# Optimization experiments

Measured on AMD Instinct MI355X. Metric: run time of the kernel, lower is better.

## Reference

```python
import jax, jax.numpy as jnp
import numpy as np

N, E, L, H, C, F, NCLASS, NGRAPH = 50000, 800000, 3, 2, 64, 128, 10, 64
NEG_SLOPE = 0.2


def setup_inputs() -> dict:
    key = jax.random.key(0)
    ks = jax.random.split(key, 8)
    x = jax.random.normal(ks[0], (N, F), dtype=jnp.float32)
    edge_index = jax.random.randint(ks[1], (2, E), 0, N, dtype=jnp.int64)
    batch = jnp.sort(jax.random.randint(ks[2], (N,), 0, NGRAPH, dtype=jnp.int64))
    s = 1.0 / np.sqrt(F)
    W = jax.random.normal(ks[3], (L, F, H * C), dtype=jnp.float32) * s
    att_src = jax.random.normal(ks[4], (L, H, C), dtype=jnp.float32) * s
    att_dst = jax.random.normal(ks[5], (L, H, C), dtype=jnp.float32) * s
    bias = jnp.zeros((L, H * C), dtype=jnp.float32)
    lin_w = jax.random.normal(ks[6], (H * C, NCLASS), dtype=jnp.float32) * s
    lin_b = jnp.zeros((NCLASS,), dtype=jnp.float32)
    return {"x": x, "edge_index": edge_index, "batch": batch, "W": W,
            "att_src": att_src, "att_dst": att_dst, "bias": bias,
            "lin_w": lin_w, "lin_b": lin_b}


def _gat_layer(x, src, dst, w, a_s, a_d, b):
    n = x.shape[0]
    h = (x @ w).reshape(n, H, C)                      # [N,H,C]
    alpha_src = jnp.sum(h * a_s, axis=-1)             # [N,H]
    alpha_dst = jnp.sum(h * a_d, axis=-1)             # [N,H]
    e = jax.nn.leaky_relu(alpha_src[src] + alpha_dst[dst], NEG_SLOPE)  # [E2,H]
    # scatter-softmax over incoming edges of each destination node
    m = jax.ops.segment_max(e, dst, num_segments=n)
    p = jnp.exp(e - m[dst])
    z = jax.ops.segment_sum(p, dst, num_segments=n)
    alpha = p / z[dst]                                # [E2,H]
    msg = h[src] * alpha[:, :, None]                  # [E2,H,C]
    out = jax.ops.segment_sum(msg, dst, num_segments=n)  # [N,H,C]
    return out.reshape(n, H * C) + b


def reference(x, edge_index, batch, W, att_src, att_dst, bias, lin_w, lin_b):
    n = x.shape[0]
    # PyG GATConv default: add self-loops
    loop = jnp.arange(n, dtype=edge_index.dtype)
    src = jnp.concatenate([edge_index[0], loop])
    dst = jnp.concatenate([edge_index[1], loop])
    for l in range(L):
        x = _gat_layer(x, src, dst, W[l], att_src[l], att_dst[l], bias[l])
        x = jax.nn.elu(x)  # activation; dropout/bn inactive (eval, use_bn=False)
    # global mean pool per graph
    sums = jax.ops.segment_sum(x, batch, num_segments=NGRAPH)
    cnt = jax.ops.segment_sum(jnp.ones((n,), x.dtype), batch, num_segments=NGRAPH)
    pooled = sums / jnp.maximum(cnt, 1.0)[:, None]    # [NGRAPH, H*C]
    logits = pooled @ lin_w + lin_b
    return jax.nn.softmax(logits, axis=1)
```

## Files before the change

### kernel.cpp

```cpp
#include <hip/hip_runtime.h>
#include <math.h>

#define NNODES 50000
#define NEDGES 800000
#define NLAYERS 3
#define NHEADS 2
#define NCH 64
#define FDIM 128
#define NCLS 10
#define NGRAPH 64
#define NEG_SLOPE 0.2f
#define NBLK ((NNODES + 255) / 256)
#define GEMMB ((NNODES + 63) / 64)
#define HISTB ((NEDGES + 255) / 256)

#define WAVE_SYNC()                      \
  do {                                   \
    __builtin_amdgcn_wave_barrier();     \
    __asm__ volatile("" ::: "memory");   \
  } while (0)

__device__ __forceinline__ unsigned short f2bf(float f) {
  unsigned int u = __builtin_bit_cast(unsigned int, f);
  unsigned int r = u + 0x7FFFu + ((u >> 16) & 1u);
  return (unsigned short)(r >> 16);
}
__device__ __forceinline__ float bflo(unsigned v) {
  return __builtin_bit_cast(float, v << 16);
}
__device__ __forceinline__ float bfhi(unsigned v) {
  return __builtin_bit_cast(float, v & 0xFFFF0000u);
}


__global__ void k_init(int* __restrict__ deg, float* __restrict__ gsum,
                       float* __restrict__ gcnt) {
  int i = blockIdx.x * 256 + threadIdx.x;
  if (i < NNODES) deg[i] = 1;
  if (i < NGRAPH * FDIM) gsum[i] = 0.f;
  if (i < NGRAPH) gcnt[i] = 0.f;
}

__global__ __launch_bounds__(256) void k_scan1(const int* __restrict__ deg,
                                               int* __restrict__ pre,
                                               int* __restrict__ bsum) {
  __shared__ int ps[256];
  int t = threadIdx.x;
  int i = blockIdx.x * 256 + t;
  int c = (i < NNODES) ? deg[i] : 0;
  ps[t] = c;
  __syncthreads();
  for (int off = 1; off < 256; off <<= 1) {
    int v = (t >= off) ? ps[t - off] : 0;
    __syncthreads();
    ps[t] += v;
    __syncthreads();
  }
  if (i < NNODES) pre[i] = ps[t] - c;
  if (t == 255) bsum[blockIdx.x] = ps[255];
}

__global__ __launch_bounds__(256) void k_scan2(const int* __restrict__ bsum,
                                               int* __restrict__ boff) {
  __shared__ int ps[256];
  int t = threadIdx.x;
  int c = (t < NBLK) ? bsum[t] : 0;
  ps[t] = c;
  __syncthreads();
  for (int off = 1; off < 256; off <<= 1) {
    int v = (t >= off) ? ps[t - off] : 0;
    __syncthreads();
    ps[t] += v;
    __syncthreads();
  }
  if (t < NBLK) boff[t] = ps[t] - c;
}

__global__ void k_scan3(const int* __restrict__ pre,
                        const int* __restrict__ boff,
                        int* __restrict__ row_ptr, int* __restrict__ csr) {
  int i = blockIdx.x * 256 + threadIdx.x;
  if (i < NNODES) {
    int o = pre[i] + boff[i >> 8];
    row_ptr[i] = o;
    csr[o] = i;
  }
  if (i == 0) row_ptr[NNODES] = NEDGES + NNODES;
}

__global__ void k_scatter(const int* __restrict__ ei,
                          const int* __restrict__ row_ptr,
                          const int* __restrict__ rank, int* __restrict__ csr) {
  int e = blockIdx.x * 256 + threadIdx.x;
  if (e < NEDGES) {
    int d = ei[NEDGES + e];
    csr[row_ptr[d] + rank[e]] = ei[e];
  }
}

__device__ __forceinline__ void gemm_body(int blk, const float* __restrict__ X,
                                          const float* __restrict__ Wg,
                                          const float* __restrict__ a_sL,
                                          const float* __restrict__ a_dL,
                                          unsigned* __restrict__ Hb,
                                          float* __restrict__ as_,
                                          float* __restrict__ ad_) {
  __shared__ float Xs[64][33];
  __shared__ float Ws[32][128];
  int t = threadIdx.x;
  int lane = t & 63;
  int row0 = blk * 64;
  int col = (t & 31) * 4;
  int rbase = (t >> 5) * 8;
  float acc[8][4];
#pragma unroll
  for (int i = 0; i < 8; ++i)
#pragma unroll
    for (int j = 0; j < 4; ++j) acc[i][j] = 0.f;

  for (int k0 = 0; k0 < 128; k0 += 32) {
    {
      int xr = t >> 2, xk = (t & 3) * 8;
      int gr = row0 + xr;
      float4 v0 = make_float4(0.f, 0.f, 0.f, 0.f), v1 = v0;
      if (gr < NNODES) {
        const float* p = X + (size_t)gr * 128 + k0 + xk;
        v0 = *(const float4*)p;
        v1 = *(const float4*)(p + 4);
      }
      Xs[xr][xk + 0] = v0.x; Xs[xr][xk + 1] = v0.y;
      Xs[xr][xk + 2] = v0.z; Xs[xr][xk + 3] = v0.w;
      Xs[xr][xk + 4] = v1.x; Xs[xr][xk + 5] = v1.y;
      Xs[xr][xk + 6] = v1.z; Xs[xr][xk + 7] = v1.w;
    }
    {
      int wr = t >> 3, wc = (t & 7) * 16;
      const float* p = Wg + (size_t)(k0 + wr) * 128 + wc;
#pragma unroll
      for (int j = 0; j < 4; ++j) {
        float4 v = *(const float4*)(p + 4 * j);
        *(float4*)&Ws[wr][wc + 4 * j] = v;
      }
    }
    __syncthreads();
#pragma unroll
    for (int kk = 0; kk < 32; ++kk) {
      float4 b = *(const float4*)&Ws[kk][col];
#pragma unroll
      for (int i = 0; i < 8; ++i) {
        float a = Xs[rbase + i][kk];
        acc[i][0] += a * b.x;
        acc[i][1] += a * b.y;
        acc[i][2] += a * b.z;
        acc[i][3] += a * b.w;
      }
    }
    __syncthreads();
  }

  float4 asv = *(const float4*)&a_sL[col];
  float4 adv = *(const float4*)&a_dL[col];
  int head = (t >> 4) & 1;
#pragma unroll
  for (int i = 0; i < 8; ++i) {
    int r = row0 + rbase + i;
    bool ok = (r < NNODES);
    float ps = acc[i][0] * asv.x + acc[i][1] * asv.y + acc[i][2] * asv.z +
               acc[i][3] * asv.w;
    float pd = acc[i][0] * adv.x + acc[i][1] * adv.y + acc[i][2] * adv.z +
               acc[i][3] * adv.w;
#pragma unroll
    for (int off = 8; off > 0; off >>= 1) {
      ps += __shfl_xor(ps, off, 64);
      pd += __shfl_xor(pd, off, 64);
    }
    if (ok && (t & 15) == 0) {
      as_[r * 2 + head] = ps;
      ad_[r * 2 + head] = pd;
    }
    unsigned pk[4];
#pragma unroll
    for (int j = 0; j < 4; ++j) {
      float hi = __shfl(acc[i][j], (lane + 16) & 63, 64);
      pk[j] = (unsigned)f2bf(acc[i][j]) | ((unsigned)f2bf(hi) << 16);
    }
    if (ok && (t & 31) < 16) {
      *(uint4*)&Hb[(size_t)r * 64 + col] =
          make_uint4(pk[0], pk[1], pk[2], pk[3]);
    }
  }
}

__global__ __launch_bounds__(256) void k_gemm(const float* __restrict__ X,
                                              const float* __restrict__ Wg,
                                              const float* __restrict__ a_sL,
                                              const float* __restrict__ a_dL,
                                              unsigned* __restrict__ Hb,
                                              float* __restrict__ as_,
                                              float* __restrict__ ad_) {
  gemm_body(blockIdx.x, X, Wg, a_sL, a_dL, Hb, as_, ad_);
}

__global__ __launch_bounds__(256) void k_front(
    const float* __restrict__ X, const float* __restrict__ Wg,
    const float* __restrict__ a_sL, const float* __restrict__ a_dL,
    unsigned* __restrict__ Hb, float* __restrict__ as_,
    float* __restrict__ ad_, const int* __restrict__ ei, int* __restrict__ deg,
    int* __restrict__ rank, const int* __restrict__ batch,
    float* __restrict__ gcnt) {
  int b = blockIdx.x;
  if (b < GEMMB) {
    gemm_body(b, X, Wg, a_sL, a_dL, Hb, as_, ad_);
  } else if (b < GEMMB + HISTB) {
    int e = (b - GEMMB) * 256 + threadIdx.x;
    if (e < NEDGES) rank[e] = atomicAdd(&deg[ei[NEDGES + e]], 1);
  } else {
    __shared__ float loc[NGRAPH];
    int t = threadIdx.x;
    if (t < NGRAPH) loc[t] = 0.f;
    __syncthreads();
    int n = (b - GEMMB - HISTB) * 256 + t;
    if (n < NNODES) atomicAdd(&loc[batch[n]], 1.f);
    __syncthreads();
    if (t < NGRAPH && loc[t] > 0.f) atomicAdd(&gcnt[t], loc[t]);
  }
}

__global__ __launch_bounds__(256) void k_aggregate(
    const unsigned* __restrict__ Hb, const float* __restrict__ as_,
    const float* __restrict__ ad_, const int* __restrict__ row_ptr,
    const int* __restrict__ csr, const float* __restrict__ bias,
    float* __restrict__ Xout) {
  __shared__ float2 wb[4][64];
  __shared__ int sb[4][64];
  int wv = threadIdx.x >> 6;
  int lane = threadIdx.x & 63;
  int node = blockIdx.x * 4 + wv;
  if (node >= NNODES) return;
  int rs = row_ptr[node], re = row_ptr[node + 1];
  float2 adv = *(const float2*)&ad_[node * 2];

  float z0 = 0.f, z1 = 0.f, acc0 = 0.f, acc1 = 0.f;
  for (int base = rs; base < re; base += 64) {
    int j = base + lane;
    float p0 = 0.f, p1 = 0.f;
    int s = 0;
    if (j < re) {
      s = csr[j];
      float2 asv = *(const float2*)&as_[s * 2];
      float e0 = asv.x + adv.x; e0 = (e0 > 0.f) ? e0 : NEG_SLOPE * e0;
      float e1 = asv.y + adv.y; e1 = (e1 > 0.f) ? e1 : NEG_SLOPE * e1;
      p0 = __expf(e0);
      p1 = __expf(e1);
    }
    z0 += p0;
    z1 += p1;
    wb[wv][lane] = make_float2(p0, p1);
    sb[wv][lane] = s;
    WAVE_SYNC();
    int cl = min(64, re - base);
    int jj = 0;
    for (; jj + 4 <= cl; jj += 4) {
      int s0 = sb[wv][jj + 0], s1 = sb[wv][jj + 1];
      int s2 = sb[wv][jj + 2], s3 = sb[wv][jj + 3];
      float2 w0 = wb[wv][jj + 0], w1 = wb[wv][jj + 1];
      float2 w2 = wb[wv][jj + 2], w3 = wb[wv][jj + 3];
      unsigned v0 = Hb[(size_t)s0 * 64 + lane];
      unsigned v1 = Hb[(size_t)s1 * 64 + lane];
      unsigned v2 = Hb[(size_t)s2 * 64 + lane];
      unsigned v3 = Hb[(size_t)s3 * 64 + lane];
      acc0 += w0.x * bflo(v0); acc1 += w0.y * bfhi(v0);
      acc0 += w1.x * bflo(v1); acc1 += w1.y * bfhi(v1);
      acc0 += w2.x * bflo(v2); acc1 += w2.y * bfhi(v2);
      acc0 += w3.x * bflo(v3); acc1 += w3.y * bfhi(v3);
    }
    for (; jj < cl; ++jj) {
      int ss = sb[wv][jj];
      float2 w = wb[wv][jj];
      unsigned v = Hb[(size_t)ss * 64 + lane];
      acc0 += w.x * bflo(v);
      acc1 += w.y * bfhi(v);
    }
    WAVE_SYNC();
  }
#pragma unroll
  for (int off = 32; off > 0; off >>= 1) {
    z0 += __shfl_xor(z0, off, 64);
    z1 += __shfl_xor(z1, off, 64);
  }
  float o0 = acc0 / z0 + bias[lane];
  float o1 = acc1 / z1 + bias[64 + lane];
  o0 = (o0 > 0.f) ? o0 : expm1f(o0);
  o1 = (o1 > 0.f) ? o1 : expm1f(o1);
  Xout[(size_t)node * 128 + lane] = o0;
  Xout[(size_t)node * 128 + 64 + lane] = o1;
}


__global__ __launch_bounds__(128) void k_pool(const float* __restrict__ Xf,
                                              const int* __restrict__ batch,
                                              float* __restrict__ gsum) {
  int c = threadIdx.x;
  int n0 = blockIdx.x * 64;
  if (n0 >= NNODES) return;
  int n1 = min(n0 + 64, NNODES);
  int cur = batch[n0];
  float acc = 0.f;
  for (int n = n0; n < n1; ++n) {
    int g = batch[n];
    if (g != cur) {
      atomicAdd(&gsum[cur * FDIM + c], acc);
      acc = 0.f;
      cur = g;
    }
    acc += Xf[(size_t)n * 128 + c];
  }
  atomicAdd(&gsum[cur * FDIM + c], acc);
}

__global__ __launch_bounds__(64) void k_final(const float* __restrict__ gsum,
                                              const float* __restrict__ gcnt,
                                              const float* __restrict__ lw,
                                              const float* __restrict__ lb,
                                              float* __restrict__ out) {
  int g = threadIdx.x;
  float inv = 1.f / fmaxf(gcnt[g], 1.f);
  float lg[NCLS];
#pragma unroll
  for (int k = 0; k < NCLS; ++k) lg[k] = lb[k];
  for (int c = 0; c < FDIM; ++c) {
    float pv = gsum[g * FDIM + c] * inv;
#pragma unroll
    for (int k = 0; k < NCLS; ++k) lg[k] += pv * lw[c * NCLS + k];
  }
  float mx = lg[0];
#pragma unroll
  for (int k = 1; k < NCLS; ++k) mx = fmaxf(mx, lg[k]);
  float s = 0.f;
#pragma unroll
  for (int k = 0; k < NCLS; ++k) {
    lg[k] = expf(lg[k] - mx);
    s += lg[k];
  }
  float invs = 1.f / s;
#pragma unroll
  for (int k = 0; k < NCLS; ++k) out[g * NCLS + k] = lg[k] * invs;
}


extern "C" void kernel_launch(void* const* d_in, const int* in_sizes, int n_in,
                              void* d_out, int out_size, void* d_ws,
                              size_t ws_size, hipStream_t stream) {
  const float* x = (const float*)d_in[0];
  const int* ei = (const int*)d_in[1];
  const int* batch = (const int*)d_in[2];
  const float* W = (const float*)d_in[3];
  const float* a_s = (const float*)d_in[4];
  const float* a_d = (const float*)d_in[5];
  const float* bias = (const float*)d_in[6];
  const float* lw = (const float*)d_in[7];
  const float* lb = (const float*)d_in[8];
  float* out = (float*)d_out;

  unsigned* Hb = (unsigned*)d_ws;
  float* xb = (float*)(Hb + (size_t)NNODES * 64);
  float* as_ = xb + (size_t)NNODES * 128;
  float* ad_ = as_ + (size_t)NNODES * 2;
  float* gsum = ad_ + (size_t)NNODES * 2;
  float* gcnt = gsum + NGRAPH * FDIM;
  int* row_ptr = (int*)(gcnt + NGRAPH);
  int* csr = row_ptr + (NNODES + 1);
  int* deg = csr + (NEDGES + NNODES);
  int* pre = deg + NNODES;
  int* bsum = pre + NNODES;
  int* boff = bsum + NBLK;
  int* rank = boff + NBLK;

  k_init<<<(NNODES + 255) / 256, 256, 0, stream>>>(deg, gsum, gcnt);
  k_front<<<GEMMB + HISTB + NBLK, 256, 0, stream>>>(
      x, W, a_s, a_d, Hb, as_, ad_, ei, deg, rank, batch, gcnt);
  k_scan1<<<NBLK, 256, 0, stream>>>(deg, pre, bsum);
  k_scan2<<<1, 256, 0, stream>>>(bsum, boff);
  k_scan3<<<NBLK, 256, 0, stream>>>(pre, boff, row_ptr, csr);
  k_scatter<<<HISTB, 256, 0, stream>>>(ei, row_ptr, rank, csr);

  for (int l = 0; l < NLAYERS; ++l) {
    if (l > 0) {
      k_gemm<<<GEMMB, 256, 0, stream>>>(xb, W + l * FDIM * FDIM,
                                        a_s + l * FDIM, a_d + l * FDIM, Hb,
                                        as_, ad_);
    }
    k_aggregate<<<(NNODES + 3) / 4, 256, 0, stream>>>(
        Hb, as_, ad_, row_ptr, csr, bias + l * FDIM, xb);
  }
  k_pool<<<(NNODES + 63) / 64, 128, 0, stream>>>(xb, batch, gsum);
  k_final<<<1, 64, 0, stream>>>(gsum, gcnt, lw, lb, out);
}
```

Measured before the change: 357.6 us.

## Use bf16 MFMA for node projection GEMM with pre-transposed bf16 weights

Replaces the scalar fp32 tiled GEMM with a bf16 MFMA 16x16x32 kernel. A new prep kernel converts and transposes W to bf16 once per call. The per-node init kernel becomes a memset, with the self-loop degree offset folded into the scan and scatter. The aggregation gather loop is unrolled to 8 edges for more memory-level parallelism. Inputs are rounded to bf16 before the matmul, which lowers accuracy of the projection.

```diff
diff --git a/kernel.cpp b/kernel.cpp
--- a/kernel.cpp
+++ b/kernel.cpp
@@ -20,6 +20,9 @@
     __asm__ volatile("" ::: "memory");   \
   } while (0)
 
+typedef __attribute__((ext_vector_type(8))) short bf16x8;
+typedef __attribute__((ext_vector_type(4))) float f32x4;
+
 __device__ __forceinline__ unsigned short f2bf(float f) {
   unsigned int u = __builtin_bit_cast(unsigned int, f);
   unsigned int r = u + 0x7FFFu + ((u >> 16) & 1u);
@@ -32,14 +35,33 @@
   return __builtin_bit_cast(float, v & 0xFFFF0000u);
 }
 
-
-__global__ void k_init(int* __restrict__ deg, float* __restrict__ gsum,
-                       float* __restrict__ gcnt) {
-  int i = blockIdx.x * 256 + threadIdx.x;
-  if (i < NNODES) deg[i] = 1;
-  if (i < NGRAPH * FDIM) gsum[i] = 0.f;
-  if (i < NGRAPH) gcnt[i] = 0.f;
-}
+__global__ __launch_bounds__(256) void k_wprep(const float* __restrict__ W,
+                                               unsigned* __restrict__ Wt) {
+  __shared__ float Lt[128][132];
+  int l = blockIdx.x;
+  const float* Wl = W + (size_t)l * FDIM * FDIM;
+  unsigned* Wtl = Wt + (size_t)l * FDIM * FDIM / 2;
+  int t = threadIdx.x;
+#pragma unroll
+  for (int i = 0; i < 16; ++i) {
+    int k = (t >> 5) + 8 * i;
+    int n4 = (t & 31) * 4;
+    float4 v = *(const float4*)(Wl + (size_t)k * 128 + n4);
+    Lt[k][n4 + 0] = v.x;
+    Lt[k][n4 + 1] = v.y;
+    Lt[k][n4 + 2] = v.z;
+    Lt[k][n4 + 3] = v.w;
+  }
+  __syncthreads();
+  int n = t >> 1;
+  int kh = (t & 1) * 64;
+  for (int kk = 0; kk < 64; kk += 2) {
+    unsigned pk = (unsigned)f2bf(Lt[kh + kk][n]) |
+                  ((unsigned)f2bf(Lt[kh + kk + 1][n]) << 16);
+    Wtl[n * 64 + (kh >> 1) + (kk >> 1)] = pk;
+  }
+}
+
 
 __global__ __launch_bounds__(256) void k_scan1(const int* __restrict__ deg,
                                                int* __restrict__ pre,
@@ -47,7 +69,7 @@
   __shared__ int ps[256];
   int t = threadIdx.x;
   int i = blockIdx.x * 256 + t;
-  int c = (i < NNODES) ? deg[i] : 0;
+  int c = (i < NNODES) ? (deg[i] + 1) : 0;
   ps[t] = c;
   __syncthreads();
   for (int off = 1; off < 256; off <<= 1) {
@@ -94,115 +116,124 @@
   int e = blockIdx.x * 256 + threadIdx.x;
   if (e < NEDGES) {
     int d = ei[NEDGES + e];
-    csr[row_ptr[d] + rank[e]] = ei[e];
+    csr[row_ptr[d] + 1 + rank[e]] = ei[e];
   }
 }
 
 __device__ __forceinline__ void gemm_body(int blk, const float* __restrict__ X,
-                                          const float* __restrict__ Wg,
+                                          const unsigned* __restrict__ Wt,
                                           const float* __restrict__ a_sL,
                                           const float* __restrict__ a_dL,
                                           unsigned* __restrict__ Hb,
                                           float* __restrict__ as_,
                                           float* __restrict__ ad_) {
-  __shared__ float Xs[64][33];
-  __shared__ float Ws[32][128];
+  __shared__ unsigned short Xs[64][136];
+  __shared__ unsigned short Wsh[128][136];
   int t = threadIdx.x;
   int lane = t & 63;
+  int w = t >> 6;
   int row0 = blk * 64;
-  int col = (t & 31) * 4;
-  int rbase = (t >> 5) * 8;
-  float acc[8][4];
-#pragma unroll
-  for (int i = 0; i < 8; ++i)
-#pragma unroll
-    for (int j = 0; j < 4; ++j) acc[i][j] = 0.f;
-
-  for (int k0 = 0; k0 < 128; k0 += 32) {
-    {
-      int xr = t >> 2, xk = (t & 3) * 8;
-      int gr = row0 + xr;
-      float4 v0 = make_float4(0.f, 0.f, 0.f, 0.f), v1 = v0;
-      if (gr < NNODES) {
-        const float* p = X + (size_t)gr * 128 + k0 + xk;
-        v0 = *(const float4*)p;
-        v1 = *(const float4*)(p + 4);
+
+  {
+    int r = t >> 2;
+    int gr = row0 + r;
+    const float* xp = X + (size_t)gr * 128;
+#pragma unroll
+    for (int i = 0; i < 8; ++i) {
+      int c4 = ((t & 3) + 4 * i) * 4;
+      float4 v = make_float4(0.f, 0.f, 0.f, 0.f);
+      if (gr < NNODES) v = *(const float4*)(xp + c4);
+      unsigned lo = (unsigned)f2bf(v.x) | ((unsigned)f2bf(v.y) << 16);
+      unsigned hi = (unsigned)f2bf(v.z) | ((unsigned)f2bf(v.w) << 16);
+      *(uint2*)&Xs[r][c4] = make_uint2(lo, hi);
+    }
+  }
+  {
+    int n = t >> 1;
+    const uint4* wp = (const uint4*)(Wt + n * 64 + (t & 1) * 32);
+    int kh = (t & 1) * 64;
+#pragma unroll
+    for (int i = 0; i < 8; ++i) {
+      uint4 v = wp[i];
+      *(uint4*)&Wsh[n][kh + i * 8] = v;
+    }
+  }
+  __syncthreads();
+
+  int n16 = lane & 15;
+  int quad = lane >> 4;
+  int m0 = w * 16;
+  f32x4 acc[8];
+#pragma unroll
+  for (int nt = 0; nt < 8; ++nt) {
+    f32x4 z = {0.f, 0.f, 0.f, 0.f};
+    acc[nt] = z;
+  }
+#pragma unroll
+  for (int kk = 0; kk < 4; ++kk) {
+    bf16x8 af = *(const bf16x8*)&Xs[m0 + n16][kk * 32 + quad * 8];
+#pragma unroll
+    for (int nt = 0; nt < 8; ++nt) {
+      bf16x8 bf = *(const bf16x8*)&Wsh[nt * 16 + n16][kk * 32 + quad * 8];
+      acc[nt] =
+          __builtin_amdgcn_mfma_f32_16x16x32_bf16(af, bf, acc[nt], 0, 0, 0);
+    }
+  }
+
+  float asv[8], adv[8];
+#pragma unroll
+  for (int nt = 0; nt < 8; ++nt) {
+    asv[nt] = a_sL[nt * 16 + n16];
+    adv[nt] = a_dL[nt * 16 + n16];
+  }
+#pragma unroll
+  for (int r = 0; r < 4; ++r) {
+    int row = row0 + m0 + quad * 4 + r;
+    bool ok = (row < NNODES);
+    float ps0 = 0.f, pd0 = 0.f, ps1 = 0.f, pd1 = 0.f;
+#pragma unroll
+    for (int nt = 0; nt < 4; ++nt) {
+      ps0 += acc[nt][r] * asv[nt];
+      pd0 += acc[nt][r] * adv[nt];
+      ps1 += acc[nt + 4][r] * asv[nt + 4];
+      pd1 += acc[nt + 4][r] * adv[nt + 4];
+    }
+#pragma unroll
+    for (int off = 1; off < 16; off <<= 1) {
+      ps0 += __shfl_xor(ps0, off, 64);
+      pd0 += __shfl_xor(pd0, off, 64);
+      ps1 += __shfl_xor(ps1, off, 64);
+      pd1 += __shfl_xor(pd1, off, 64);
+    }
+    if (ok && n16 == 0) {
+      as_[row * 2 + 0] = ps0;
+      as_[row * 2 + 1] = ps1;
+      ad_[row * 2 + 0] = pd0;
+      ad_[row * 2 + 1] = pd1;
+    }
+    if (ok) {
+#pragma unroll
+      for (int nt = 0; nt < 4; ++nt) {
+        unsigned pk = (unsigned)f2bf(acc[nt][r]) |
+                      ((unsigned)f2bf(acc[nt + 4][r]) << 16);
+        Hb[(size_t)row * 64 + nt * 16 + n16] = pk;
       }
-      Xs[xr][xk + 0] = v0.x; Xs[xr][xk + 1] = v0.y;
-      Xs[xr][xk + 2] = v0.z; Xs[xr][xk + 3] = v0.w;
-      Xs[xr][xk + 4] = v1.x; Xs[xr][xk + 5] = v1.y;
-      Xs[xr][xk + 6] = v1.z; Xs[xr][xk + 7] = v1.w;
-    }
-    {
-      int wr = t >> 3, wc = (t & 7) * 16;
-      const float* p = Wg + (size_t)(k0 + wr) * 128 + wc;
-#pragma unroll
-      for (int j = 0; j < 4; ++j) {
-        float4 v = *(const float4*)(p + 4 * j);
-        *(float4*)&Ws[wr][wc + 4 * j] = v;
-      }
-    }
-    __syncthreads();
-#pragma unroll
-    for (int kk = 0; kk < 32; ++kk) {
-      float4 b = *(const float4*)&Ws[kk][col];
-#pragma unroll
-      for (int i = 0; i < 8; ++i) {
-        float a = Xs[rbase + i][kk];
-        acc[i][0] += a * b.x;
-        acc[i][1] += a * b.y;
-        acc[i][2] += a * b.z;
-        acc[i][3] += a * b.w;
-      }
-    }
-    __syncthreads();
-  }
-
-  float4 asv = *(const float4*)&a_sL[col];
-  float4 adv = *(const float4*)&a_dL[col];
-  int head = (t >> 4) & 1;
-#pragma unroll
-  for (int i = 0; i < 8; ++i) {
-    int r = row0 + rbase + i;
-    bool ok = (r < NNODES);
-    float ps = acc[i][0] * asv.x + acc[i][1] * asv.y + acc[i][2] * asv.z +
-               acc[i][3] * asv.w;
-    float pd = acc[i][0] * adv.x + acc[i][1] * adv.y + acc[i][2] * adv.z +
-               acc[i][3] * adv.w;
-#pragma unroll
-    for (int off = 8; off > 0; off >>= 1) {
-      ps += __shfl_xor(ps, off, 64);
-      pd += __shfl_xor(pd, off, 64);
-    }
-    if (ok && (t & 15) == 0) {
-      as_[r * 2 + head] = ps;
-      ad_[r * 2 + head] = pd;
-    }
-    unsigned pk[4];
-#pragma unroll
-    for (int j = 0; j < 4; ++j) {
-      float hi = __shfl(acc[i][j], (lane + 16) & 63, 64);
-      pk[j] = (unsigned)f2bf(acc[i][j]) | ((unsigned)f2bf(hi) << 16);
-    }
-    if (ok && (t & 31) < 16) {
-      *(uint4*)&Hb[(size_t)r * 64 + col] =
-          make_uint4(pk[0], pk[1], pk[2], pk[3]);
     }
   }
 }
 
 __global__ __launch_bounds__(256) void k_gemm(const float* __restrict__ X,
-                                              const float* __restrict__ Wg,
+                                              const unsigned* __restrict__ Wt,
                                               const float* __restrict__ a_sL,
                                               const float* __restrict__ a_dL,
                                               unsigned* __restrict__ Hb,
                                               float* __restrict__ as_,
                                               float* __restrict__ ad_) {
-  gemm_body(blockIdx.x, X, Wg, a_sL, a_dL, Hb, as_, ad_);
+  gemm_body(blockIdx.x, X, Wt, a_sL, a_dL, Hb, as_, ad_);
 }
 
 __global__ __launch_bounds__(256) void k_front(
-    const float* __restrict__ X, const float* __restrict__ Wg,
+    const float* __restrict__ X, const unsigned* __restrict__ Wt,
     const float* __restrict__ a_sL, const float* __restrict__ a_dL,
     unsigned* __restrict__ Hb, float* __restrict__ as_,
     float* __restrict__ ad_, const int* __restrict__ ei, int* __restrict__ deg,
@@ -210,7 +241,7 @@
     float* __restrict__ gcnt) {
   int b = blockIdx.x;
   if (b < GEMMB) {
-    gemm_body(b, X, Wg, a_sL, a_dL, Hb, as_, ad_);
+    gemm_body(b, X, Wt, a_sL, a_dL, Hb, as_, ad_);
   } else if (b < GEMMB + HISTB) {
     int e = (b - GEMMB) * 256 + threadIdx.x;
     if (e < NEDGES) rank[e] = atomicAdd(&deg[ei[NEDGES + e]], 1);
@@ -239,6 +270,7 @@
   if (node >= NNODES) return;
   int rs = row_ptr[node], re = row_ptr[node + 1];
   float2 adv = *(const float2*)&ad_[node * 2];
+  const unsigned* Hl = Hb + lane;
 
   float z0 = 0.f, z1 = 0.f, acc0 = 0.f, acc1 = 0.f;
   for (int base = rs; base < re; base += 64) {
@@ -260,24 +292,31 @@
     WAVE_SYNC();
     int cl = min(64, re - base);
     int jj = 0;
-    for (; jj + 4 <= cl; jj += 4) {
-      int s0 = sb[wv][jj + 0], s1 = sb[wv][jj + 1];
-      int s2 = sb[wv][jj + 2], s3 = sb[wv][jj + 3];
+    for (; jj + 8 <= cl; jj += 8) {
+      unsigned v0 = Hl[(size_t)sb[wv][jj + 0] * 64];
+      unsigned v1 = Hl[(size_t)sb[wv][jj + 1] * 64];
+      unsigned v2 = Hl[(size_t)sb[wv][jj + 2] * 64];
+      unsigned v3 = Hl[(size_t)sb[wv][jj + 3] * 64];
+      unsigned v4 = Hl[(size_t)sb[wv][jj + 4] * 64];
+      unsigned v5 = Hl[(size_t)sb[wv][jj + 5] * 64];
+      unsigned v6 = Hl[(size_t)sb[wv][jj + 6] * 64];
+      unsigned v7 = Hl[(size_t)sb[wv][jj + 7] * 64];
       float2 w0 = wb[wv][jj + 0], w1 = wb[wv][jj + 1];
       float2 w2 = wb[wv][jj + 2], w3 = wb[wv][jj + 3];
-      unsigned v0 = Hb[(size_t)s0 * 64 + lane];
-      unsigned v1 = Hb[(size_t)s1 * 64 + lane];
-      unsigned v2 = Hb[(size_t)s2 * 64 + lane];
-      unsigned v3 = Hb[(size_t)s3 * 64 + lane];
+      float2 w4 = wb[wv][jj + 4], w5 = wb[wv][jj + 5];
+      float2 w6 = wb[wv][jj + 6], w7 = wb[wv][jj + 7];
       acc0 += w0.x * bflo(v0); acc1 += w0.y * bfhi(v0);
       acc0 += w1.x * bflo(v1); acc1 += w1.y * bfhi(v1);
       acc0 += w2.x * bflo(v2); acc1 += w2.y * bfhi(v2);
       acc0 += w3.x * bflo(v3); acc1 += w3.y * bfhi(v3);
+      acc0 += w4.x * bflo(v4); acc1 += w4.y * bfhi(v4);
+      acc0 += w5.x * bflo(v5); acc1 += w5.y * bfhi(v5);
+      acc0 += w6.x * bflo(v6); acc1 += w6.y * bfhi(v6);
+      acc0 += w7.x * bflo(v7); acc1 += w7.y * bfhi(v7);
     }
     for (; jj < cl; ++jj) {
-      int ss = sb[wv][jj];
+      unsigned v = Hl[(size_t)sb[wv][jj] * 64];
       float2 w = wb[wv][jj];
-      unsigned v = Hb[(size_t)ss * 64 + lane];
       acc0 += w.x * bflo(v);
       acc1 += w.y * bfhi(v);
     }
@@ -368,17 +407,19 @@
   float* ad_ = as_ + (size_t)NNODES * 2;
   float* gsum = ad_ + (size_t)NNODES * 2;
   float* gcnt = gsum + NGRAPH * FDIM;
-  int* row_ptr = (int*)(gcnt + NGRAPH);
+  int* deg = (int*)(gcnt + NGRAPH);
+  int* row_ptr = deg + NNODES;
   int* csr = row_ptr + (NNODES + 1);
-  int* deg = csr + (NEDGES + NNODES);
-  int* pre = deg + NNODES;
+  int* pre = csr + (NEDGES + NNODES);
   int* bsum = pre + NNODES;
   int* boff = bsum + NBLK;
   int* rank = boff + NBLK;
-
-  k_init<<<(NNODES + 255) / 256, 256, 0, stream>>>(deg, gsum, gcnt);
+  unsigned* Wt = (unsigned*)(rank + NEDGES);
+
+  hipMemsetAsync(gsum, 0, (NGRAPH * FDIM + NGRAPH + NNODES) * 4, stream);
+  k_wprep<<<NLAYERS, 256, 0, stream>>>(W, Wt);
   k_front<<<GEMMB + HISTB + NBLK, 256, 0, stream>>>(
-      x, W, a_s, a_d, Hb, as_, ad_, ei, deg, rank, batch, gcnt);
+      x, Wt, a_s, a_d, Hb, as_, ad_, ei, deg, rank, batch, gcnt);
   k_scan1<<<NBLK, 256, 0, stream>>>(deg, pre, bsum);
   k_scan2<<<1, 256, 0, stream>>>(bsum, boff);
   k_scan3<<<NBLK, 256, 0, stream>>>(pre, boff, row_ptr, csr);
@@ -386,7 +427,7 @@
 
   for (int l = 0; l < NLAYERS; ++l) {
     if (l > 0) {
-      k_gemm<<<GEMMB, 256, 0, stream>>>(xb, W + l * FDIM * FDIM,
+      k_gemm<<<GEMMB, 256, 0, stream>>>(xb, Wt + (size_t)l * FDIM * FDIM / 2,
                                         a_s + l * FDIM, a_d + l * FDIM, Hb,
                                         as_, ad_);
     }
```

Result: faster. 334.6 us (-6.4%).
